# Kernel tuning notes

Hardware: AMD Instinct MI355X
Metric: run time of the kernel (lower is better)

Reference implementation:

```python
import jax, jax.numpy as jnp
import numpy as np

B, T, N = 1024, 5, 6        # batch, seq_len (fixed by conv3d1 kernel), max_node_num
D, E, M, L = 192, 12, 12, 512  # node feat, edge feat, message size, link hidden
P = 2                        # propagate_layers
O = 6                        # big_attr_classes / conv3d out channels


def setup_inputs() -> dict:
    key = jax.random.key(0)
    ks = jax.random.split(key, 16)
    w = lambda k, shp: jax.random.normal(k, shp, jnp.float32) * 0.02
    return {
        "node_resnet": jax.random.normal(ks[0], (B, T, D, N), jnp.float32),
        "pos": jax.random.normal(ks[1], (B, T, N, 6), jnp.float32),
        "attmat": jax.random.randint(ks[2], (B, T, N, N), 0, 2).astype(jnp.int32),
        "link_w1": w(ks[3], (L, E)), "link_b1": jnp.zeros((L,), jnp.float32),
        "link_w2": w(ks[4], (1, L)), "link_b2": jnp.zeros((1,), jnp.float32),
        "msg_Wh": w(ks[5], (M, D)), "msg_We": w(ks[6], (M, E)), "msg_b": jnp.zeros((M,), jnp.float32),
        "gru_Wih": w(ks[7], (3 * D, M)), "gru_Whh": w(ks[8], (3 * D, D)),
        "gru_bih": jnp.zeros((3 * D,), jnp.float32), "gru_bhh": jnp.zeros((3 * D,), jnp.float32),
        "conv1_w": w(ks[9], (O, D, T, N, 1)), "conv1_b": jnp.zeros((O,), jnp.float32),
        "conv2_w": w(ks[10], (O, O)), "conv2_b": jnp.zeros((O,), jnp.float32),
    }


def reference(node_resnet, pos, attmat, link_w1, link_b1, link_w2, link_b2,
              msg_Wh, msg_We, msg_b, gru_Wih, gru_Whh, gru_bih, gru_bhh,
              conv1_w, conv1_b, conv2_w, conv2_b):
    # edge features: e[b,t,:,i,j] = cat(pos_i, pos_j) where ATTMAT==1 and i!=j
    eye = jnp.eye(N, dtype=bool)
    mask = (attmat == 1) & (~eye)[None, None]                      # [B,T,N,N]
    pi = jnp.broadcast_to(pos[:, :, :, None, :], (B, T, N, N, 6))
    pj = jnp.broadcast_to(pos[:, :, None, :, :], (B, T, N, N, 6))
    e = jnp.concatenate([pi, pj], -1) * mask[..., None]            # [B,T,N,N,E]
    e = jnp.moveaxis(e, -1, 2)                                     # [B,T,E,N,N]

    def link(es):  # GraphConv link function: 1x1 conv stack -> scalar edge logit
        hmid = jax.nn.relu(jnp.einsum('btcij,oc->btoij', es, link_w1)
                           + link_b1[None, None, :, None, None])
        return jnp.einsum('btoij,po->btpij', hmid, link_w2)[:, :, 0] + link_b2[0]  # [B,T,N,N]

    h = node_resnet                                                # [B,T,D,N]
    edge_state = e
    for _ in range(P):
        adj = jax.nn.sigmoid(link(edge_state))                     # [B,T,N,N] gate (i=target, j=source)
        # message: relu(Wh h_j + We e_ij + b), gated by sigmoid adjacency
        mh = jnp.einsum('btcj,oc->btoj', h, msg_Wh)                # [B,T,M,N]
        me = jnp.einsum('btcij,oc->btoij', e, msg_We)              # [B,T,M,N,N]
        m = jax.nn.relu(mh[:, :, :, None, :] + me + msg_b[None, None, :, None, None])
        m = adj[:, :, None, :, :] * m                              # gated messages
        edge_state = m                                             # next-round edge hidden state
        msum = m.sum(-1)                                           # aggregate over source j: [B,T,M,N]
        # GRU update per node (PyTorch gate order r, z, n)
        x = jnp.moveaxis(msum, 2, -1)                              # [B,T,N,M]
        hh = jnp.moveaxis(h, 2, -1)                                # [B,T,N,D]
        gi = x @ gru_Wih.T + gru_bih
        gh = hh @ gru_Whh.T + gru_bhh
        ir, iz, inn = jnp.split(gi, 3, -1)
        hr, hz, hn = jnp.split(gh, 3, -1)
        r = jax.nn.sigmoid(ir + hr)
        z = jax.nn.sigmoid(iz + hz)
        n = jnp.tanh(inn + r * hn)
        hh = (1.0 - z) * n + z * hh
        h = jnp.moveaxis(hh, -1, 2)                                # [B,T,D,N]

    # conv3d1 kernel (5,6,1) spans full (T,N) -> single contraction per batch
    out = jax.nn.relu(jnp.einsum('btdn,odtn->bo', h, conv1_w[..., 0]) + conv1_b)
    out = out @ conv2_w.T + conv2_b                                # conv3d2 is 1x1x1
    return out.reshape(B, O, 1, 1, 1)
```

## Files before the change

### kernel.cpp

```cpp
#include <hip/hip_runtime.h>
#include <math.h>

#define NB 1024
#define TT 5
#define NN 6
#define DD 192
#define EE 12
#define MM 12
#define LL 512
#define OO 6
#define GOUT 768
#define KPAD 224
#define NKT (KPAD/32)
#define NJT (GOUT/16)
#define ROWS 30
#define HP 196
#define GRUPU 116

typedef __attribute__((ext_vector_type(8))) _Float16 f16x8;
typedef __attribute__((ext_vector_type(2))) _Float16 h2;
typedef __attribute__((ext_vector_type(4))) float f32x4;

__device__ __forceinline__ float dot4(float4 a, float4 b) {
  return a.x*b.x + a.y*b.y + a.z*b.z + a.w*b.w;
}
__device__ __forceinline__ unsigned short f2h(float f) {
  _Float16 h = (_Float16)f;
  unsigned short s; __builtin_memcpy(&s, &h, 2); return s;
}
__device__ __forceinline__ float h2f(unsigned short s) {
  _Float16 h; __builtin_memcpy(&h, &s, 2); return (float)h;
}
__device__ __forceinline__ unsigned int pkrtz(float a, float b) {
  auto v = __builtin_amdgcn_cvt_pkrtz(a, b);
  return __builtin_bit_cast(unsigned int, v);
}
__device__ __forceinline__ float fsig(float x) {
  float e = __expf(-x);
  return __builtin_amdgcn_rcpf(1.f + e);
}
__device__ __forceinline__ float ftanh(float x) {
  float e = __expf(-2.f * x);
  return 2.f * __builtin_amdgcn_rcpf(1.f + e) - 1.f;
}

__global__ void k_pack(const float* __restrict__ Wih, const float* __restrict__ Whh,
                       const float* __restrict__ bih, const float* __restrict__ bhh,
                       unsigned short* __restrict__ Bh, float* __restrict__ bias768)
{
  int idx = blockIdx.x * 256 + threadIdx.x;
  if (idx < GOUT) {
    int c = idx; float b;
    if (c < 384)      b = bih[c] + bhh[c];
    else if (c < 576) b = bih[c];
    else              b = bhh[c - 192];
    bias768[c] = b;
  }
  if (idx >= NJT*NKT*512) return;
  int e = idx & 7, l = (idx >> 3) & 63;
  int rem = idx >> 9, kt = rem % NKT, j = rem / NKT;
  int k = kt*32 + ((l >> 4) << 3) + e;
  int c = j*16 + (l & 15);
  float v = 0.f;
  if (k < 204) {
    if (c < 384)      v = (k < 12) ? Wih[c*MM + k] : Whh[(size_t)c*DD + (k-12)];
    else if (c < 576) v = (k < 12) ? Wih[c*MM + k] : 0.f;
    else              v = (k < 12) ? 0.f : Whh[(size_t)(c-192)*DD + (k-12)];
  }
  Bh[idx] = f2h(v);
}

__global__ void k_pack_link(const float* __restrict__ w1,
                            unsigned short* __restrict__ BLh)
{
  int idx = blockIdx.x * 256 + threadIdx.x;
  if (idx >= 32*512) return;
  int e = idx & 7, l = (idx >> 3) & 63, nt = idx >> 9;
  int k = ((l >> 4) << 3) + e;
  int c = nt*16 + (l & 15);
  BLh[idx] = f2h((k < 12) ? w1[c*EE + k] : 0.f);
}

__global__ __launch_bounds__(256, 2)
void k_fused(const float* __restrict__ nr, const float* __restrict__ pos,
             const int* __restrict__ attmat,
             const unsigned short* __restrict__ BLh,
             const float* __restrict__ lb1, const float* __restrict__ lw2,
             const float* __restrict__ lb2,
             const float* __restrict__ msg_Wh, const float* __restrict__ msg_We,
             const float* __restrict__ msg_b,
             const unsigned short* __restrict__ Bh, const float* __restrict__ bias768,
             const float* __restrict__ conv1_w, const float* __restrict__ conv1_b,
             const float* __restrict__ conv2_w, const float* __restrict__ conv2_b,
             float* __restrict__ out)
{
  __shared__ __align__(16) float sh_h[ROWS][HP];
  __shared__ __align__(16) unsigned int sh_e[180][6];
  __shared__ __align__(16) unsigned int sh_m[180][6];
  __shared__ __align__(16) unsigned int shA[16*GRUPU];
  __shared__ __align__(16) unsigned short sh_mh[ROWS][MM];
  __shared__ __align__(16) unsigned int sh_we[MM][6];
  __shared__ unsigned short sh_adj[180];

  const int tid = threadIdx.x;
  const int b = blockIdx.x;
  const int lane = tid & 63, wid = tid >> 6;
  const int col = lane & 15, quad = lane >> 4;

  for (int i = tid; i < TT*DD*NN; i += 256) {
    int t = i / (DD*NN), rem = i % (DD*NN);
    int d = rem / NN, n = rem % NN;
    sh_h[t*NN + n][d] = nr[(size_t)b*TT*DD*NN + i];
  }
  for (int idx = tid; idx < 180*6; idx += 256) {
    int e = idx / 6, p = idx % 6;
    int t = e / 36, ij = e % 36;
    int i_ = ij / NN, j_ = ij % NN;
    bool msk = (attmat[(b*TT + t)*36 + ij] == 1) && (i_ != j_);
    int srcn = (p < 3) ? i_ : j_;
    int c0   = (p < 3) ? 2*p : 2*p - 6;
    const float* pb = pos + (((size_t)(b*TT + t))*NN + srcn)*6;
    float a0 = msk ? pb[c0] : 0.f, a1 = msk ? pb[c0+1] : 0.f;
    sh_e[e][p] = pkrtz(a0, a1);
  }
  for (int idx = tid; idx < MM*6; idx += 256) {
    int o = idx / 6, p = idx % 6;
    sh_we[o][p] = pkrtz(msg_We[o*EE + 2*p], msg_We[o*EE + 2*p + 1]);
  }
  __syncthreads();

  for (int L = 0; L < 2; ++L) {
    {
      f16x8 am[3];
      #pragma unroll
      for (int mtl = 0; mtl < 3; ++mtl) {
        int r = (wid*3 + mtl)*16 + col; r = r > 179 ? 179 : r;
        const unsigned int* src = (L == 0) ? &sh_e[r][0] : &sh_m[r][0];
        uint4 w = make_uint4(0u, 0u, 0u, 0u);
        if (quad == 0) {
          uint2 lo = *(const uint2*)(src);
          uint2 hi = *(const uint2*)(src + 2);
          w = make_uint4(lo.x, lo.y, hi.x, hi.y);
        } else if (quad == 1) {
          uint2 lo = *(const uint2*)(src + 4);
          w = make_uint4(lo.x, lo.y, 0u, 0u);
        }
        am[mtl] = __builtin_bit_cast(f16x8, w);
      }
      float s[3][4];
      #pragma unroll
      for (int mtl = 0; mtl < 3; ++mtl)
        #pragma unroll
        for (int q = 0; q < 4; ++q) s[mtl][q] = 0.f;
      for (int nt = 0; nt < 32; ++nt) {
        f16x8 bh = *(const f16x8*)(BLh + nt*512 + lane*8);
        float b1v = lb1[nt*16 + col];
        float w2v = lw2[nt*16 + col];
        #pragma unroll
        for (int mtl = 0; mtl < 3; ++mtl) {
          f32x4 acc = (f32x4)0.f;
          acc = __builtin_amdgcn_mfma_f32_16x16x32_f16(am[mtl], bh, acc, 0, 0, 0);
          #pragma unroll
          for (int q = 0; q < 4; ++q)
            s[mtl][q] += w2v * fmaxf(acc[q] + b1v, 0.f);
        }
      }
      #pragma unroll
      for (int mtl = 0; mtl < 3; ++mtl)
        #pragma unroll
        for (int q = 0; q < 4; ++q) {
          float v = s[mtl][q];
          v += __shfl_xor(v, 1); v += __shfl_xor(v, 2);
          v += __shfl_xor(v, 4); v += __shfl_xor(v, 8);
          s[mtl][q] = v;
        }
      if (col == 0) {
        float b2 = lb2[0];
        #pragma unroll
        for (int mtl = 0; mtl < 3; ++mtl)
          #pragma unroll
          for (int q = 0; q < 4; ++q) {
            int e = wid*48 + mtl*16 + quad*4 + q;
            if (e < 180) sh_adj[e] = f2h(fsig(s[mtl][q] + b2));
          }
      }
    }
    __syncthreads();

    for (int idx = tid; idx < ROWS*MM; idx += 256) {
      int r = idx / MM, o = idx % MM;
      const float4* wrow = (const float4*)(msg_Wh + (size_t)o*DD);
      const float4* hrow = (const float4*)&sh_h[r][0];
      float acc = msg_b[o];
      #pragma unroll 8
      for (int d4 = 0; d4 < DD/4; ++d4) acc += dot4(wrow[d4], hrow[d4]);
      sh_mh[r][o] = f2h(acc);
    }
    __syncthreads();

    for (int idx = tid; idx < 180*6; idx += 256) {
      int e = idx / 6, op = idx % 6;
      int t = e / 36, j_ = e % 6;
      h2 a2 = {(_Float16)0.f, (_Float16)0.f};
      h2 b2 = {(_Float16)0.f, (_Float16)0.f};
      #pragma unroll
      for (int p = 0; p < 6; ++p) {
        h2 ev = __builtin_bit_cast(h2, sh_e[e][p]);
        a2 += __builtin_bit_cast(h2, sh_we[2*op][p]) * ev;
        b2 += __builtin_bit_cast(h2, sh_we[2*op+1][p]) * ev;
      }
      float me0 = (float)a2[0] + (float)a2[1];
      float me1 = (float)b2[0] + (float)b2[1];
      float mh0 = h2f(sh_mh[t*NN + j_][2*op]);
      float mh1 = h2f(sh_mh[t*NN + j_][2*op + 1]);
      float adj = h2f(sh_adj[e]);
      sh_m[e][op] = pkrtz(adj * fmaxf(mh0 + me0, 0.f),
                          adj * fmaxf(mh1 + me1, 0.f));
    }
    __syncthreads();

    #pragma unroll 1
    for (int H = 0; H < 2; ++H) {
      for (int idx = tid; idx < 16*(KPAD/2); idx += 256) {
        int r = idx / (KPAD/2), kp = idx % (KPAD/2);
        int grow = H*16 + r;
        unsigned int v = 0;
        if (grow < ROWS) {
          if (kp < 6) {
            int t = grow / NN, i_ = grow % NN;
            const unsigned int* mrow = &sh_m[t*36 + i_*NN][kp];
            float a0 = 0.f, a1 = 0.f;
            #pragma unroll
            for (int j = 0; j < 6; ++j) {
              h2 mv = __builtin_bit_cast(h2, mrow[j*6]);
              a0 += (float)mv[0]; a1 += (float)mv[1];
            }
            v = pkrtz(a0, a1);
          } else if (kp < 102) {
            float2 hv = *(const float2*)&sh_h[grow][2*kp - 12];
            v = pkrtz(hv.x, hv.y);
          }
        }
        shA[r*GRUPU + kp] = v;
      }
      __syncthreads();

      {
        const char* ahb = (const char*)shA + col*(GRUPU*4) + quad*16;
        #pragma unroll 1
        for (int i = 0; i < 3; ++i) {
          const int jR = wid*3 + i;
          const int jZ = 12 + wid*3 + i;
          const int jI = 24 + wid*3 + i;
          const int jH = 36 + wid*3 + i;
          f32x4 aR = (f32x4)0.f, aZ = (f32x4)0.f;
          f32x4 aI = (f32x4)0.f, aH = (f32x4)0.f;
          #pragma unroll
          for (int kt = 0; kt < NKT; ++kt) {
            f16x8 ah = *(const f16x8*)(ahb + kt*64);
            f16x8 bR = *(const f16x8*)(Bh + (((size_t)(jR*NKT + kt)) << 9) + lane*8);
            f16x8 bZ = *(const f16x8*)(Bh + (((size_t)(jZ*NKT + kt)) << 9) + lane*8);
            f16x8 bH = *(const f16x8*)(Bh + (((size_t)(jH*NKT + kt)) << 9) + lane*8);
            aR = __builtin_amdgcn_mfma_f32_16x16x32_f16(ah, bR, aR, 0, 0, 0);
            aZ = __builtin_amdgcn_mfma_f32_16x16x32_f16(ah, bZ, aZ, 0, 0, 0);
            aH = __builtin_amdgcn_mfma_f32_16x16x32_f16(ah, bH, aH, 0, 0, 0);
            if (kt == 0) {
              f16x8 bI = *(const f16x8*)(Bh + (((size_t)(jI*NKT)) << 9) + lane*8);
              aI = __builtin_amdgcn_mfma_f32_16x16x32_f16(ah, bI, aI, 0, 0, 0);
            }
          }
          const int d = (wid*3 + i)*16 + col;
          const float bR_ = bias768[d],       bZ_ = bias768[192 + d];
          const float bI_ = bias768[384 + d], bH_ = bias768[576 + d];
          #pragma unroll
          for (int q = 0; q < 4; ++q) {
            const int grow = H*16 + quad*4 + q;
            if (grow < ROWS) {
              float r_ = fsig(aR[q] + bR_);
              float z_ = fsig(aZ[q] + bZ_);
              float n_ = ftanh(aI[q] + bI_ + r_*(aH[q] + bH_));
              float hold = sh_h[grow][d];
              sh_h[grow][d] = (1.f - z_)*n_ + z_*hold;
            }
          }
        }
      }
      __syncthreads();
    }
  }

  {
    float* red = (float*)&sh_mh[0][0];
    float acco[OO];
    #pragma unroll
    for (int o = 0; o < OO; ++o) acco[o] = 0.f;
    for (int u = tid; u < DD*TT*NN; u += 256) {
      int r = u % ROWS, c = u / ROWS;
      float hv = sh_h[r][c];
      #pragma unroll
      for (int o = 0; o < OO; ++o)
        acco[o] += conv1_w[o*(DD*TT*NN) + u] * hv;
    }
    #pragma unroll
    for (int o = 0; o < OO; ++o) {
      float v = acco[o];
      v += __shfl_xor(v, 1);  v += __shfl_xor(v, 2);  v += __shfl_xor(v, 4);
      v += __shfl_xor(v, 8);  v += __shfl_xor(v, 16); v += __shfl_xor(v, 32);
      acco[o] = v;
    }
    __syncthreads();
    if (lane == 0) {
      #pragma unroll
      for (int o = 0; o < OO; ++o) red[wid*OO + o] = acco[o];
    }
    __syncthreads();
    if (tid == 0) {
      float y[OO];
      #pragma unroll
      for (int o = 0; o < OO; ++o) {
        float s = conv1_b[o] + red[0*OO+o] + red[1*OO+o] + red[2*OO+o] + red[3*OO+o];
        y[o] = fmaxf(s, 0.f);
      }
      #pragma unroll
      for (int q = 0; q < OO; ++q) {
        float s = conv2_b[q];
        #pragma unroll
        for (int o = 0; o < OO; ++o) s += conv2_w[q*OO + o] * y[o];
        out[b*OO + q] = s;
      }
    }
  }
}

extern "C" void kernel_launch(void* const* d_in, const int* in_sizes, int n_in,
                              void* d_out, int out_size, void* d_ws, size_t ws_size,
                              hipStream_t stream) {
  const float* node_resnet = (const float*)d_in[0];
  const float* pos      = (const float*)d_in[1];
  const int*   attmat   = (const int*)  d_in[2];
  const float* link_w1  = (const float*)d_in[3];
  const float* link_b1  = (const float*)d_in[4];
  const float* link_w2  = (const float*)d_in[5];
  const float* link_b2  = (const float*)d_in[6];
  const float* msg_Wh   = (const float*)d_in[7];
  const float* msg_We   = (const float*)d_in[8];
  const float* msg_b    = (const float*)d_in[9];
  const float* gru_Wih  = (const float*)d_in[10];
  const float* gru_Whh  = (const float*)d_in[11];
  const float* gru_bih  = (const float*)d_in[12];
  const float* gru_bhh  = (const float*)d_in[13];
  const float* conv1_w  = (const float*)d_in[14];
  const float* conv1_b  = (const float*)d_in[15];
  const float* conv2_w  = (const float*)d_in[16];
  const float* conv2_b  = (const float*)d_in[17];
  float* out = (float*)d_out;

  float* bias = (float*)d_ws;
  unsigned short* Bh  = (unsigned short*)(bias + GOUT);
  unsigned short* BLh = Bh + (size_t)NJT*NKT*512;

  k_pack<<<(NJT*NKT*512 + 255)/256, 256, 0, stream>>>(gru_Wih, gru_Whh,
      gru_bih, gru_bhh, Bh, bias);
  k_pack_link<<<(32*512 + 255)/256, 256, 0, stream>>>(link_w1, BLh);
  k_fused<<<NB, 256, 0, stream>>>(node_resnet, pos, attmat,
      BLh, link_b1, link_w2, link_b2,
      msg_Wh, msg_We, msg_b,
      Bh, bias,
      conv1_w, conv1_b, conv2_w, conv2_b, out);
}
```

Before: 142.1 us.

## Fold link bias and |w2| into weights, use 16x16x16 MFMA for link

Rescales the link layer-1 weights by |w2| and folds b1 in as an extra K column, fed by a constant 1.0 in the A operand. relu(a*x) = a*relu(x) for a>0, so the inner loop reduces to a sign-weighted fma. This shrinks K from 32 to 16, switching to the 16x16x16 f16 MFMA and halving B-operand loads. The per-iteration b1/w2 loads and add are dropped. One __syncthreads between the link stage and the msg_Wh projection is also removed; the two stages write disjoint buffers. Folding the bias into fp16 weights adds a small rounding risk.

```diff
diff --git a/kernel.cpp b/kernel.cpp
--- a/kernel.cpp
+++ b/kernel.cpp
@@ -18,6 +18,7 @@
 #define GRUPU 116
 
 typedef __attribute__((ext_vector_type(8))) _Float16 f16x8;
+typedef __attribute__((ext_vector_type(4))) _Float16 f16x4;
 typedef __attribute__((ext_vector_type(2))) _Float16 h2;
 typedef __attribute__((ext_vector_type(4))) float f32x4;
 
@@ -70,23 +71,29 @@
   Bh[idx] = f2h(v);
 }
 
-__global__ void k_pack_link(const float* __restrict__ w1,
-                            unsigned short* __restrict__ BLh)
+__global__ void k_pack_link(const float* __restrict__ w1, const float* __restrict__ b1,
+                            const float* __restrict__ w2,
+                            unsigned short* __restrict__ BLh16,
+                            float* __restrict__ lsgn)
 {
   int idx = blockIdx.x * 256 + threadIdx.x;
-  if (idx >= 32*512) return;
-  int e = idx & 7, l = (idx >> 3) & 63, nt = idx >> 9;
-  int k = ((l >> 4) << 3) + e;
+  if (idx < LL) lsgn[idx] = (w2[idx] < 0.f) ? -1.f : 1.f;
+  if (idx >= 32*256) return;
+  int e = idx & 3, l = (idx >> 2) & 63, nt = idx >> 8;
+  int k = ((l >> 4) << 2) + e;
   int c = nt*16 + (l & 15);
-  BLh[idx] = f2h((k < 12) ? w1[c*EE + k] : 0.f);
+  float aw = fabsf(w2[c]);
+  float v = 0.f;
+  if (k < 12)       v = aw * w1[c*EE + k];
+  else if (k == 12) v = aw * b1[c];
+  BLh16[idx] = f2h(v);
 }
 
 __global__ __launch_bounds__(256, 2)
 void k_fused(const float* __restrict__ nr, const float* __restrict__ pos,
              const int* __restrict__ attmat,
-             const unsigned short* __restrict__ BLh,
-             const float* __restrict__ lb1, const float* __restrict__ lw2,
-             const float* __restrict__ lb2,
+             const unsigned short* __restrict__ BLh16,
+             const float* __restrict__ lsgn, const float* __restrict__ lb2,
              const float* __restrict__ msg_Wh, const float* __restrict__ msg_We,
              const float* __restrict__ msg_b,
              const unsigned short* __restrict__ Bh, const float* __restrict__ bias768,
@@ -131,21 +138,17 @@
 
   for (int L = 0; L < 2; ++L) {
     {
-      f16x8 am[3];
+      f16x4 am[3];
       #pragma unroll
       for (int mtl = 0; mtl < 3; ++mtl) {
         int r = (wid*3 + mtl)*16 + col; r = r > 179 ? 179 : r;
         const unsigned int* src = (L == 0) ? &sh_e[r][0] : &sh_m[r][0];
-        uint4 w = make_uint4(0u, 0u, 0u, 0u);
-        if (quad == 0) {
-          uint2 lo = *(const uint2*)(src);
-          uint2 hi = *(const uint2*)(src + 2);
-          w = make_uint4(lo.x, lo.y, hi.x, hi.y);
-        } else if (quad == 1) {
-          uint2 lo = *(const uint2*)(src + 4);
-          w = make_uint4(lo.x, lo.y, 0u, 0u);
-        }
-        am[mtl] = __builtin_bit_cast(f16x8, w);
+        uint2 w;
+        if (quad == 0)      w = *(const uint2*)(src);
+        else if (quad == 1) w = *(const uint2*)(src + 2);
+        else if (quad == 2) w = *(const uint2*)(src + 4);
+        else                w = make_uint2(0x00003C00u, 0u);
+        am[mtl] = __builtin_bit_cast(f16x4, w);
       }
       float s[3][4];
       #pragma unroll
@@ -153,16 +156,15 @@
         #pragma unroll
         for (int q = 0; q < 4; ++q) s[mtl][q] = 0.f;
       for (int nt = 0; nt < 32; ++nt) {
-        f16x8 bh = *(const f16x8*)(BLh + nt*512 + lane*8);
-        float b1v = lb1[nt*16 + col];
-        float w2v = lw2[nt*16 + col];
+        f16x4 bh = *(const f16x4*)(BLh16 + nt*256 + lane*4);
+        float sg = lsgn[nt*16 + col];
         #pragma unroll
         for (int mtl = 0; mtl < 3; ++mtl) {
           f32x4 acc = (f32x4)0.f;
-          acc = __builtin_amdgcn_mfma_f32_16x16x32_f16(am[mtl], bh, acc, 0, 0, 0);
+          acc = __builtin_amdgcn_mfma_f32_16x16x16f16(am[mtl], bh, acc, 0, 0, 0);
           #pragma unroll
           for (int q = 0; q < 4; ++q)
-            s[mtl][q] += w2v * fmaxf(acc[q] + b1v, 0.f);
+            s[mtl][q] = fmaf(sg, fmaxf(acc[q], 0.f), s[mtl][q]);
         }
       }
       #pragma unroll
@@ -184,17 +186,15 @@
             if (e < 180) sh_adj[e] = f2h(fsig(s[mtl][q] + b2));
           }
       }
-    }
-    __syncthreads();
-
-    for (int idx = tid; idx < ROWS*MM; idx += 256) {
-      int r = idx / MM, o = idx % MM;
-      const float4* wrow = (const float4*)(msg_Wh + (size_t)o*DD);
-      const float4* hrow = (const float4*)&sh_h[r][0];
-      float acc = msg_b[o];
-      #pragma unroll 8
-      for (int d4 = 0; d4 < DD/4; ++d4) acc += dot4(wrow[d4], hrow[d4]);
-      sh_mh[r][o] = f2h(acc);
+      for (int idx = tid; idx < ROWS*MM; idx += 256) {
+        int r = idx / MM, o = idx % MM;
+        const float4* wrow = (const float4*)(msg_Wh + (size_t)o*DD);
+        const float4* hrow = (const float4*)&sh_h[r][0];
+        float acc = msg_b[o];
+        #pragma unroll 8
+        for (int d4 = 0; d4 < DD/4; ++d4) acc += dot4(wrow[d4], hrow[d4]);
+        sh_mh[r][o] = f2h(acc);
+      }
     }
     __syncthreads();
 
@@ -356,14 +356,16 @@
   float* out = (float*)d_out;
 
   float* bias = (float*)d_ws;
-  unsigned short* Bh  = (unsigned short*)(bias + GOUT);
-  unsigned short* BLh = Bh + (size_t)NJT*NKT*512;
+  unsigned short* Bh    = (unsigned short*)(bias + GOUT);
+  unsigned short* BLh16 = Bh + (size_t)NJT*NKT*512;
+  float* lsgn = (float*)(BLh16 + (size_t)32*256);
 
   k_pack<<<(NJT*NKT*512 + 255)/256, 256, 0, stream>>>(gru_Wih, gru_Whh,
       gru_bih, gru_bhh, Bh, bias);
-  k_pack_link<<<(32*512 + 255)/256, 256, 0, stream>>>(link_w1, BLh);
+  k_pack_link<<<(32*256 + 255)/256, 256, 0, stream>>>(link_w1, link_b1, link_w2,
+      BLh16, lsgn);
   k_fused<<<NB, 256, 0, stream>>>(node_resnet, pos, attmat,
-      BLh, link_b1, link_w2, link_b2,
+      BLh16, lsgn, link_b2,
       msg_Wh, msg_We, msg_b,
       Bh, bias,
       conv1_w, conv1_b, conv2_w, conv2_b, out);
```

Result: slower. 156.8 us (+10.3%).
